# Optimization experiments

Hardware: AMD Instinct MI355X
Metric: run time of the kernel (lower is better)

The kernel has to match this reference:

```python
import jax, jax.numpy as jnp
import numpy as np
import math

NUM_HEADS = 16
HEAD_DIM = 64

def setup_inputs() -> dict:
    key = jax.random.key(0)
    k1, = jax.random.split(key, 1)
    x = jax.random.normal(k1, (4, 4096, NUM_HEADS, HEAD_DIM), dtype=jnp.float32)
    log_amp = jnp.zeros((NUM_HEADS,), dtype=jnp.float32)
    log_decay = jnp.full((NUM_HEADS,), math.log(0.3), dtype=jnp.float32)
    mix_logit = jnp.zeros((NUM_HEADS,), dtype=jnp.float32)
    return {"x": x, "log_amp": log_amp, "log_decay": log_decay, "mix_logit": mix_logit}

def _next_power_of_two(v: int) -> int:
    return 1 << (v - 1).bit_length()

def reference(x, log_amp, log_decay, mix_logit):
    B, L, H, D = x.shape
    n_fft = _next_power_of_two(2 * L)  # 8192 for L=4096
    # b l h d -> b h d l
    xf = jnp.transpose(x, (0, 2, 3, 1)).astype(jnp.float32)
    F = jnp.fft.rfft(xf, n=n_fft, axis=-1)  # [B,H,D,n_fft//2+1] complex64
    freq = jnp.arange(F.shape[-1], dtype=jnp.float32)
    amp = jax.nn.softplus(log_amp)[None, :, None, None]
    decay = jax.nn.softplus(log_decay)[None, :, None, None] + 1e-4
    # minimum-phase power-law filter: |H| = amp/(1+w^2)^(decay/2), phase = -decay*atan(w)
    mag = amp / jnp.power(1.0 + freq * freq, decay * 0.5)
    phase = -decay * jnp.arctan(freq)
    filt = (mag * jnp.cos(phase) + 1j * (mag * jnp.sin(phase))).astype(F.dtype)
    y = jnp.fft.irfft(F * filt, n=n_fft, axis=-1)[..., :L]
    y = jnp.transpose(y, (0, 3, 1, 2)).astype(x.dtype)  # b h d l -> b l h d
    mix = jax.nn.sigmoid(mix_logit)[None, None, :, None]
    return mix * y + (1.0 - mix) * x
```

## Files before the change

kernel.cpp:

```cpp
#include <hip/hip_runtime.h>
#include <math.h>

namespace {
constexpr int kB = 4;
constexpr int kL = 4096;
constexpr int kH = 16;
constexpr int kD = 64;
constexpr int kC = kH * kD;
constexpr int kM = 4096;
constexpr int kN2 = kL / 2;
constexpr int NTH = 256;
constexpr int kTabIters = 9;

__device__ __forceinline__ float2 cmul(float2 a, float2 b) {
  return make_float2(a.x * b.x - a.y * b.y, a.x * b.y + a.y * b.x);
}
__device__ __forceinline__ float2 cadd(float2 a, float2 b) { return make_float2(a.x + b.x, a.y + b.y); }
__device__ __forceinline__ float2 csub(float2 a, float2 b) { return make_float2(a.x - b.x, a.y - b.y); }
__device__ __forceinline__ float2 cconj(float2 a) { return make_float2(a.x, -a.y); }
__device__ __forceinline__ float2 cmuli(float2 a) { return make_float2(-a.y, a.x); }
__device__ __forceinline__ float2 cscale(float2 a, float s) { return make_float2(a.x * s, a.y * s); }

typedef float cplx __attribute__((ext_vector_type(2)));

__device__ __forceinline__ cplx pk_add(cplx a, cplx b) {
  cplx r;
  asm("v_pk_add_f32 %0, %1, %2" : "=v"(r) : "v"(a), "v"(b));
  return r;
}
__device__ __forceinline__ cplx pk_sub(cplx a, cplx b) {
  cplx r;
  asm("v_pk_add_f32 %0, %1, %2 neg_lo:[0,1] neg_hi:[0,1]" : "=v"(r) : "v"(a), "v"(b));
  return r;
}
__device__ __forceinline__ cplx pk_addpi(cplx a, cplx b) {
  cplx r;
  asm("v_pk_add_f32 %0, %1, %2 op_sel:[0,1] op_sel_hi:[1,0] neg_lo:[0,1]" : "=v"(r) : "v"(a), "v"(b));
  return r;
}
__device__ __forceinline__ cplx pk_addmi(cplx a, cplx b) {
  cplx r;
  asm("v_pk_add_f32 %0, %1, %2 op_sel:[0,1] op_sel_hi:[1,0] neg_hi:[0,1]" : "=v"(r) : "v"(a), "v"(b));
  return r;
}
__device__ __forceinline__ cplx pk_cmul(cplx a, cplx b) {
  cplx t, r;
  asm("v_pk_mul_f32 %0, %1, %2 op_sel:[0,0] op_sel_hi:[0,1]" : "=v"(t) : "v"(a), "v"(b));
  asm("v_pk_fma_f32 %0, %1, %2, %3 op_sel:[1,1,0] op_sel_hi:[1,0,1] neg_lo:[0,1,0]"
      : "=v"(r) : "v"(a), "v"(b), "v"(t));
  return r;
}

__device__ __forceinline__ unsigned pkbf(float lo, float hi) {
  unsigned r;
  asm("v_cvt_pk_bf16_f32 %0, %1, %2" : "=v"(r) : "v"(lo), "v"(hi));
  return r;
}
__device__ __forceinline__ cplx unpk(unsigned d) {
  cplx r;
  r.x = __uint_as_float(d << 16);
  r.y = __uint_as_float(d & 0xffff0000u);
  return r;
}

__device__ __forceinline__ unsigned dr4(unsigned p) {
  unsigned r = __brev(p) >> 20;
  return ((r & 0x555u) << 1) | ((r >> 1) & 0x555u);
}
__device__ __forceinline__ unsigned dr16(unsigned p) {
  return ((p & 15u) << 8) | (p & 0xF0u) | (p >> 8);
}
__device__ __forceinline__ int SW(int i) { return i ^ ((i >> 4) & 15); }
#define POS(k) ((((k) & 3) << 2) | ((k) >> 2))

__device__ __forceinline__ int IDX(int i) { return i + (i >> 4); }
constexpr int kZPad = kM + (kM >> 4);

#define TW_TREE(w)                                                            \
  cplx W1 = (w), W2 = pk_cmul(W1, W1), W4 = pk_cmul(W2, W2),                  \
       W8 = pk_cmul(W4, W4);                                                  \
  cplx W3 = pk_cmul(W2, W1), W5 = pk_cmul(W4, W1), W6 = pk_cmul(W4, W2),      \
       W7 = pk_cmul(W4, W3);                                                  \
  cplx W9 = pk_cmul(W8, W1), W10 = pk_cmul(W8, W2), W11 = pk_cmul(W8, W3),    \
       W12 = pk_cmul(W8, W4);                                                 \
  cplx W13 = pk_cmul(W8, W5), W14 = pk_cmul(W8, W6), W15 = pk_cmul(W8, W7);

#define TW_APPLY(r)                                                           \
  r[POS(1)] = pk_cmul(r[POS(1)], W1);   r[POS(2)] = pk_cmul(r[POS(2)], W2);   \
  r[POS(3)] = pk_cmul(r[POS(3)], W3);   r[POS(4)] = pk_cmul(r[POS(4)], W4);   \
  r[POS(5)] = pk_cmul(r[POS(5)], W5);   r[POS(6)] = pk_cmul(r[POS(6)], W6);   \
  r[POS(7)] = pk_cmul(r[POS(7)], W7);   r[POS(8)] = pk_cmul(r[POS(8)], W8);   \
  r[POS(9)] = pk_cmul(r[POS(9)], W9);   r[POS(10)] = pk_cmul(r[POS(10)], W10);\
  r[POS(11)] = pk_cmul(r[POS(11)], W11); r[POS(12)] = pk_cmul(r[POS(12)], W12);\
  r[POS(13)] = pk_cmul(r[POS(13)], W13); r[POS(14)] = pk_cmul(r[POS(14)], W14);\
  r[POS(15)] = pk_cmul(r[POS(15)], W15);

#define TWS_TREE(b0, w)                                                       \
  cplx P2 = pk_cmul(w, w), P4 = pk_cmul(P2, P2), P8 = pk_cmul(P4, P4);        \
  cplx B0 = (b0), B1 = pk_cmul(b0, w), B2 = pk_cmul(B0, P2),                  \
       B3 = pk_cmul(B1, P2);                                                  \
  cplx B4 = pk_cmul(B0, P4), B5 = pk_cmul(B1, P4), B6 = pk_cmul(B2, P4),      \
       B7 = pk_cmul(B3, P4);                                                  \
  cplx B8 = pk_cmul(B0, P8), B9 = pk_cmul(B1, P8), B10 = pk_cmul(B2, P8),     \
       B11 = pk_cmul(B3, P8);                                                 \
  cplx B12 = pk_cmul(B4, P8), B13 = pk_cmul(B5, P8), B14 = pk_cmul(B6, P8),   \
       B15 = pk_cmul(B7, P8);

#define TWS_APPLY(r)                                                          \
  r[POS(0)] = pk_cmul(r[POS(0)], B0);   r[POS(1)] = pk_cmul(r[POS(1)], B1);   \
  r[POS(2)] = pk_cmul(r[POS(2)], B2);   r[POS(3)] = pk_cmul(r[POS(3)], B3);   \
  r[POS(4)] = pk_cmul(r[POS(4)], B4);   r[POS(5)] = pk_cmul(r[POS(5)], B5);   \
  r[POS(6)] = pk_cmul(r[POS(6)], B6);   r[POS(7)] = pk_cmul(r[POS(7)], B7);   \
  r[POS(8)] = pk_cmul(r[POS(8)], B8);   r[POS(9)] = pk_cmul(r[POS(9)], B9);   \
  r[POS(10)] = pk_cmul(r[POS(10)], B10); r[POS(11)] = pk_cmul(r[POS(11)], B11);\
  r[POS(12)] = pk_cmul(r[POS(12)], B12); r[POS(13)] = pk_cmul(r[POS(13)], B13);\
  r[POS(14)] = pk_cmul(r[POS(14)], B14); r[POS(15)] = pk_cmul(r[POS(15)], B15);

__device__ __forceinline__ float2 filt_val(float k, float ampS, float dec) {
  float mag = ampS * __expf(-0.5f * dec * log1pf(k * k));
  float ph = -dec * atanf(k);
  float s, c;
  __sincosf(ph, &s, &c);
  return make_float2(mag * c, mag * s);
}

template <int S, bool HZ>
__device__ __forceinline__ void fft16(cplx r[16]) {
  constexpr float C1 = 0.92387953251128674f;
  constexpr float S1 = 0.38268343236508978f;
  constexpr float R2 = 0.70710678118654752f;
  const float sg = (float)S;
  const cplx Wa = {C1, sg * S1};
  const cplx Wb = {R2, sg * R2};
  const cplx Wc = {S1, sg * C1};
  const cplx Wd = {-R2, sg * R2};
  const cplx We = {-C1, -sg * S1};
#pragma unroll
  for (int n2 = 0; n2 < 4; ++n2) {
    cplx t0, t1, t2, t3;
    if (HZ) {
      t0 = r[n2]; t1 = r[n2]; t2 = r[n2 + 4]; t3 = r[n2 + 4];
    } else {
      cplx a0 = r[n2], a1 = r[n2 + 4], a2 = r[n2 + 8], a3 = r[n2 + 12];
      t0 = pk_add(a0, a2); t1 = pk_sub(a0, a2); t2 = pk_add(a1, a3); t3 = pk_sub(a1, a3);
    }
    cplx u0 = pk_add(t0, t2);
    cplx u2 = pk_sub(t0, t2);
    cplx u1 = (S < 0) ? pk_addmi(t1, t3) : pk_addpi(t1, t3);
    cplx u3 = (S < 0) ? pk_addpi(t1, t3) : pk_addmi(t1, t3);
    if (n2 == 0) { r[0] = u0; r[4] = u1; r[8] = u2; r[12] = u3; }
    if (n2 == 1) { r[1] = u0; r[5] = pk_cmul(u1, Wa); r[9] = pk_cmul(u2, Wb); r[13] = pk_cmul(u3, Wc); }
    if (n2 == 2) {
      r[2] = u0; r[6] = pk_cmul(u1, Wb);
      cplx m;
      if (S < 0) { m.x = u2.y; m.y = -u2.x; } else { m.x = -u2.y; m.y = u2.x; }
      r[10] = m;
      r[14] = pk_cmul(u3, Wd);
    }
    if (n2 == 3) { r[3] = u0; r[7] = pk_cmul(u1, Wc); r[11] = pk_cmul(u2, Wd); r[15] = pk_cmul(u3, We); }
  }
#pragma unroll
  for (int s = 0; s < 4; ++s) {
    cplx b0 = r[4 * s], b1 = r[4 * s + 1], b2 = r[4 * s + 2], b3 = r[4 * s + 3];
    cplx t0 = pk_add(b0, b2), t1 = pk_sub(b0, b2), t2 = pk_add(b1, b3), t3 = pk_sub(b1, b3);
    r[4 * s] = pk_add(t0, t2);
    r[4 * s + 2] = pk_sub(t0, t2);
    r[4 * s + 1] = (S < 0) ? pk_addmi(t1, t3) : pk_addpi(t1, t3);
    r[4 * s + 3] = (S < 0) ? pk_addpi(t1, t3) : pk_addmi(t1, t3);
  }
}

__device__ __forceinline__ void pw_pair(float2 Zk, float2 Zmk, int k, float ampS, float dec,
                                        float2* Wk, float2* Wmk) {
  float2 A = cscale(cadd(Zk, cconj(Zmk)), 0.5f);
  float2 Bv = cscale(csub(Zk, cconj(Zmk)), 0.5f);
  float sn, cs;
  __sincosf(-3.14159265358979323846f * (float)k / (float)kM, &sn, &cs);
  float2 tw = make_float2(cs, sn);
  float2 P = cmuli(cmul(tw, Bv));
  float2 Xk = csub(A, P);
  float2 Xmk = cconj(cadd(A, P));
  float2 Yk = cmul(Xk, filt_val((float)k, ampS, dec));
  float2 Ymk = cmul(Xmk, filt_val((float)(kM - k), ampS, dec));
  float2 Ev = cscale(cadd(Yk, cconj(Ymk)), 0.5f);
  float2 Ov = cscale(cmul(cconj(tw), csub(Yk, cconj(Ymk))), 0.5f);
  float2 iO = cmuli(Ov);
  *Wk = cadd(Ev, iO);
  *Wmk = cconj(csub(Ev, iO));
}
}

__global__ __launch_bounds__(256) void build_table(const float* __restrict__ la,
                                                   const float* __restrict__ ld,
                                                   float2* __restrict__ tab) {
  const int i = blockIdx.x;
  const int h = blockIdx.y;
  const int t = threadIdx.x;
  float av = la[h], dv = ld[h];
  float amp = (av > 20.f) ? av : log1pf(__expf(av));
  float dec = ((dv > 20.f) ? dv : log1pf(__expf(dv))) + 1e-4f;
  float ampS = amp * (1.0f / (float)kM);
  float2 e0 = make_float2(0.f, 0.f), e1 = e0, e2 = e0, e3 = e0;
  const int c = t & 15;
  if (i == 0 && t == 0) {
    float F0 = filt_val(0.f, ampS, dec).x;
    float FM = filt_val((float)kM, ampS, dec).x;
    e0 = make_float2(0.5f * (F0 + FM), 0.5f * (F0 - FM));
    e1 = make_float2(0.5f * (F0 - FM), 0.5f * (F0 + FM));
  } else if (i == 0 && t == 8) {
    e0 = cconj(filt_val((float)(kM / 2), ampS, dec));
  } else if ((i >= 1 && i <= 7) || c < 8) {
    int p = (i << 8) + t;
    int k = (int)dr16((unsigned)p);
    float2 a, b, g, d;
    pw_pair(make_float2(1.f, 0.f), make_float2(0.f, 0.f), k, ampS, dec, &a, &g);
    pw_pair(make_float2(0.f, 0.f), make_float2(1.f, 0.f), k, ampS, dec, &b, &d);
    e0 = a; e1 = b; e2 = g; e3 = d;
  }
  float2* e = tab + ((size_t)(h * kTabIters + i) * 256 + t) * 4;
  e[0] = e0; e[1] = e1; e[2] = e2; e[3] = e3;
}

__global__ __launch_bounds__(256) void transpose_fwd(const float* __restrict__ in,
                                                     unsigned* __restrict__ zout) {
  __shared__ float T[64][33];
  const int b = blockIdx.z;
  const int l0 = blockIdx.x * 64;
  const int c0 = blockIdx.y * 32;
  const float* ib = in + (size_t)b * kL * kC;
  unsigned* ob = zout + (size_t)b * kC * kN2;
  const int tx = threadIdx.x & 31, ty = threadIdx.x >> 5;
#pragma unroll
  for (int i = 0; i < 64; i += 8)
    T[ty + i][tx] = ib[(size_t)(l0 + ty + i) * kC + c0 + tx];
  __syncthreads();
  const int n0 = l0 >> 1;
#pragma unroll
  for (int i = 0; i < 32; i += 8) {
    int c = ty + i;
    ob[(size_t)(c0 + c) * kN2 + n0 + tx] = pkbf(T[2 * tx][c], T[2 * tx + 1][c]);
  }
}

__global__ __launch_bounds__(NTH) void fft_rows(unsigned* __restrict__ zio,
                                                const float2* __restrict__ tab) {
  __shared__ cplx Z[kM];
  const int row = blockIdx.x;
  const int h = (row >> 6) & (kH - 1);
  const int t = threadIdx.x;
  unsigned* zrow = zio + (size_t)row * kN2;

  cplx r[16];
  const int swt = t ^ ((t >> 4) & 15);

  {
    unsigned din[8];
#pragma unroll
    for (int j = 0; j < 8; ++j) din[j] = zrow[t + (j << 8)];
#pragma unroll
    for (int j = 0; j < 8; ++j) r[j] = unpk(din[j]);
    fft16<-1, true>(r);
    float sn, cs;
    __sincosf(-6.283185307179586f * (float)t / 4096.f, &sn, &cs);
    cplx w = {cs, sn};
    TW_TREE(w);
    TW_APPLY(r);
    cplx* Zb = &Z[swt];
#pragma unroll
    for (int k1 = 0; k1 < 16; ++k1) Zb[k1 << 8] = r[POS(k1)];
  }
  __syncthreads();

  {
    const int g = t >> 4, m2 = t & 15;
    const int base = g << 8;
#pragma unroll
    for (int m1 = 0; m1 < 16; ++m1) r[m1] = Z[base + (m1 << 4) + (m2 ^ m1)];
    fft16<-1, false>(r);
    float sn, cs;
    __sincosf(-6.283185307179586f * (float)m2 / 256.f, &sn, &cs);
    cplx w = {cs, sn};
    TW_TREE(w);
    TW_APPLY(r);
#pragma unroll
    for (int j1 = 0; j1 < 16; ++j1) Z[base + (j1 << 4) + (m2 ^ j1)] = r[POS(j1)];
  }
  __syncthreads();

  {
    const int g = t >> 4, j1 = t & 15;
    const int base = (g << 8) + (j1 << 4);
#pragma unroll
    for (int m2 = 0; m2 < 16; ++m2) r[m2] = Z[base + (m2 ^ j1)];
    fft16<-1, false>(r);
#pragma unroll
    for (int j2 = 0; j2 < 16; ++j2) Z[base + (j2 ^ j1)] = r[POS(j2)];
  }
  __syncthreads();

  {
    const int c = t & 15;
    const float4* tpz = (const float4*)(tab + (size_t)h * kTabIters * 256 * 4);
#pragma unroll
    for (int i = 0; i <= 8; ++i) {
      const float4* tp = tpz + ((i << 8) + t) * 2;
      float4 q0 = tp[0], q1 = tp[1];
      if (i == 0 && t == 0) {
        cplx Z0 = Z[0];
        cplx o; o.x = q0.x * Z0.x + q0.y * Z0.y; o.y = q0.z * Z0.x + q0.w * Z0.y;
        Z[0] = o;
      } else if (i == 0 && t == 8) {
        cplx f; f.x = q0.x; f.y = q0.y;
        Z[8] = pk_cmul(f, Z[8]);
      } else if ((i >= 1 && i <= 7) || c < 8) {
        int p = (i << 8) + t;
        int p2 = (i == 0) ? ((t < 16) ? (16 - t) : (271 - t))
                          : (((16 - i) << 8) + (255 - t));
        int sp = SW(p), sp2 = SW(p2);
        cplx Zk = Z[sp], Zmk = Z[sp2];
        cplx e0 = {q0.x, q0.y}, e1 = {q0.z, q0.w};
        cplx e2 = {q1.x, q1.y}, e3 = {q1.z, q1.w};
        cplx cZk = {Zk.x, -Zk.y}, cZmk = {Zmk.x, -Zmk.y};
        Z[sp] = pk_add(pk_cmul(e0, Zk), pk_cmul(e1, cZmk));
        Z[sp2] = pk_add(pk_cmul(e2, cZk), pk_cmul(e3, Zmk));
      }
    }
  }
  __syncthreads();

  {
    const int k1 = t >> 4, j1 = t & 15;
    const int base = (k1 << 8) + (j1 << 4);
#pragma unroll
    for (int j2 = 0; j2 < 16; ++j2) r[j2] = Z[base + (j2 ^ j1)];
    fft16<1, false>(r);
    float sn, cs;
    __sincosf(6.283185307179586f * (float)j1 / 256.f, &sn, &cs);
    cplx w = {cs, sn};
    TW_TREE(w);
    TW_APPLY(r);
#pragma unroll
    for (int m2 = 0; m2 < 16; ++m2) Z[base + (m2 ^ j1)] = r[POS(m2)];
  }
  __syncthreads();

  {
    const int k1 = t >> 4, m2 = t & 15;
#pragma unroll
    for (int j1 = 0; j1 < 16; ++j1) r[j1] = Z[(k1 << 8) + (j1 << 4) + (m2 ^ j1)];
    fft16<1, false>(r);
    float sn, cs;
    __sincosf(6.283185307179586f * (float)(k1 * m2) / 4096.f, &sn, &cs);
    cplx b0 = {cs, sn};
    __sincosf(6.283185307179586f * (float)k1 / 256.f, &sn, &cs);
    cplx w = {cs, sn};
    TWS_TREE(b0, w);
    TWS_APPLY(r);
#pragma unroll
    for (int m1 = 0; m1 < 16; ++m1) Z[(k1 << 8) + (m1 << 4) + (m2 ^ m1)] = r[POS(m1)];
  }
  __syncthreads();

  {
    cplx* Zb = &Z[swt];
#pragma unroll
    for (int k1 = 0; k1 < 16; ++k1) r[k1] = Zb[k1 << 8];
    fft16<1, false>(r);
#pragma unroll
    for (int n1 = 0; n1 < 8; ++n1) {
      cplx v = r[POS(n1)];
      zrow[(n1 << 8) + t] = pkbf(v.x, v.y);
    }
  }
}

__global__ __launch_bounds__(256) void mix_out(const unsigned* __restrict__ zin,
                                               const float* __restrict__ x,
                                               const float* __restrict__ mix_logit,
                                               float* __restrict__ outp) {
  __shared__ float T[64][33];
  const int b = blockIdx.z;
  const int l0 = blockIdx.x * 64;
  const int c0 = blockIdx.y * 32;
  const int h = c0 >> 6;
  const float ml = mix_logit[h];
  const float mix = 1.0f / (1.0f + __expf(-ml));
  const float omix = 1.0f - mix;
  const unsigned* yb = zin + (size_t)b * kC * kN2;
  const float* xb = x + (size_t)b * kL * kC;
  float* ob = outp + (size_t)b * kL * kC;
  const int tx = threadIdx.x & 31, ty = threadIdx.x >> 5;
  const int n0 = l0 >> 1;
#pragma unroll
  for (int i = 0; i < 32; i += 8) {
    int c = ty + i;
    unsigned d = yb[(size_t)(c0 + c) * kN2 + n0 + tx];
    T[2 * tx][c] = __uint_as_float(d << 16);
    T[2 * tx + 1][c] = __uint_as_float(d & 0xffff0000u);
  }
  __syncthreads();
#pragma unroll
  for (int i = 0; i < 64; i += 8) {
    int l = ty + i;
    size_t idx = (size_t)(l0 + l) * kC + c0 + tx;
    ob[idx] = mix * T[l][tx] + omix * xb[idx];
  }
}

__global__ __launch_bounds__(NTH) void fftconv_fallback(
    const float* __restrict__ x, const float* __restrict__ log_amp,
    const float* __restrict__ log_decay, const float* __restrict__ mix_logit,
    float* __restrict__ out) {
  __shared__ float2 Z[kZPad];
  const int row = blockIdx.x;
  const int d = row & (kD - 1);
  const int h = (row >> 6) & (kH - 1);
  const int b = row >> 10;
  const int t = threadIdx.x;
  const size_t rowoff = (size_t)b * kL * kC + (size_t)h * kD + (size_t)d;
  const float* xrow = x + rowoff;
  float* orow = out + rowoff;

  const float av = log_amp[h];
  const float dv = log_decay[h];
  const float amp = (av > 20.f) ? av : log1pf(__expf(av));
  const float dec = ((dv > 20.f) ? dv : log1pf(__expf(dv))) + 1e-4f;
  const float ampS = amp * (1.0f / (float)kM);
  const float ml = mix_logit[h];
  const float mix = 1.0f / (1.0f + __expf(-ml));
  const float omix = 1.0f - mix;

  for (int i = 0; i < kM / NTH; ++i) {
    int n = t + i * NTH;
    float2 z;
    if (n < kL / 2) {
      z.x = xrow[(size_t)(2 * n) * kC];
      z.y = xrow[(size_t)(2 * n + 1) * kC];
    } else {
      z = make_float2(0.f, 0.f);
    }
    Z[IDX(n)] = z;
  }
  __syncthreads();

  for (int Ls = kM; Ls >= 4; Ls >>= 2) {
    const int q = Ls >> 2;
    const float wstep = -6.283185307179586f / (float)Ls;
    for (int i = 0; i < kM / 4 / NTH; ++i) {
      int bt = t + i * NTH;
      int jj = bt & (q - 1);
      int base = ((bt - jj) << 2) + jj;
      float2 a = Z[IDX(base)], bb = Z[IDX(base + q)];
      float2 c = Z[IDX(base + 2 * q)], dd = Z[IDX(base + 3 * q)];
      float2 t0 = cadd(a, c), t1 = csub(a, c), t2 = cadd(bb, dd), t3 = csub(bb, dd);
      float2 u0 = cadd(t0, t2), u2 = csub(t0, t2);
      float2 it3 = cmuli(t3);
      float2 u1 = csub(t1, it3), u3 = cadd(t1, it3);
      float sn, cs;
      __sincosf(wstep * (float)jj, &sn, &cs);
      float2 w1 = make_float2(cs, sn);
      float2 w2 = cmul(w1, w1);
      float2 w3 = cmul(w2, w1);
      Z[IDX(base)] = u0;
      Z[IDX(base + q)] = cmul(u1, w1);
      Z[IDX(base + 2 * q)] = cmul(u2, w2);
      Z[IDX(base + 3 * q)] = cmul(u3, w3);
    }
    __syncthreads();
  }

  for (int i = 0; i <= kM / 2 / NTH; ++i) {
    int k = t + i * NTH;
    if (k > kM / 2) continue;
    if (k == 0) {
      float2 Z0 = Z[IDX(0)];
      float X0 = Z0.x + Z0.y;
      float XM = Z0.x - Z0.y;
      float2 f0 = filt_val(0.f, ampS, dec);
      float2 fM = filt_val((float)kM, ampS, dec);
      float Y0 = X0 * f0.x;
      float YM = XM * fM.x;
      Z[IDX(0)] = make_float2(0.5f * (Y0 + YM), 0.5f * (Y0 - YM));
    } else if (k == kM / 2) {
      unsigned p = dr4(kM / 2);
      float2 Zk = Z[IDX(p)];
      float2 f = filt_val((float)(kM / 2), ampS, dec);
      float2 Y = cmul(cconj(Zk), f);
      Z[IDX(p)] = cconj(Y);
    } else {
      unsigned pk = dr4((unsigned)k), pmk = dr4((unsigned)(kM - k));
      float2 Zk = Z[IDX(pk)], Zmk = Z[IDX(pmk)];
      float2 A = cscale(cadd(Zk, cconj(Zmk)), 0.5f);
      float2 Bv = cscale(csub(Zk, cconj(Zmk)), 0.5f);
      float sn, cs;
      __sincosf(-3.14159265358979323846f * (float)k / (float)kM, &sn, &cs);
      float2 tw = make_float2(cs, sn);
      float2 P = cmuli(cmul(tw, Bv));
      float2 Xk = csub(A, P);
      float2 Xmk = cconj(cadd(A, P));
      float2 Yk = cmul(Xk, filt_val((float)k, ampS, dec));
      float2 Ymk = cmul(Xmk, filt_val((float)(kM - k), ampS, dec));
      float2 Ev = cscale(cadd(Yk, cconj(Ymk)), 0.5f);
      float2 Ov = cscale(cmul(cconj(tw), csub(Yk, cconj(Ymk))), 0.5f);
      float2 iO = cmuli(Ov);
      Z[IDX(pk)] = cadd(Ev, iO);
      Z[IDX(pmk)] = cconj(csub(Ev, iO));
    }
  }
  __syncthreads();

  for (int Ls = 4; Ls <= kM; Ls <<= 2) {
    const int q = Ls >> 2;
    const float wstep = 6.283185307179586f / (float)Ls;
    for (int i = 0; i < kM / 4 / NTH; ++i) {
      int bt = t + i * NTH;
      int jj = bt & (q - 1);
      int base = ((bt - jj) << 2) + jj;
      float sn, cs;
      __sincosf(wstep * (float)jj, &sn, &cs);
      float2 w1 = make_float2(cs, sn);
      float2 w2 = cmul(w1, w1);
      float2 w3 = cmul(w2, w1);
      float2 a = Z[IDX(base)];
      float2 bb = cmul(Z[IDX(base + q)], w1);
      float2 c = cmul(Z[IDX(base + 2 * q)], w2);
      float2 dd = cmul(Z[IDX(base + 3 * q)], w3);
      float2 s0 = cadd(a, c), s1 = csub(a, c), s2 = cadd(bb, dd), s3 = csub(bb, dd);
      float2 is3 = cmuli(s3);
      Z[IDX(base)] = cadd(s0, s2);
      Z[IDX(base + 2 * q)] = csub(s0, s2);
      Z[IDX(base + q)] = cadd(s1, is3);
      Z[IDX(base + 3 * q)] = csub(s1, is3);
    }
    __syncthreads();
  }

  for (int i = 0; i < kL / 2 / NTH; ++i) {
    int n = t + i * NTH;
    float2 w = Z[IDX(n)];
    size_t i0 = (size_t)(2 * n) * kC;
    float x0 = xrow[i0];
    float x1 = xrow[i0 + kC];
    orow[i0] = mix * w.x + omix * x0;
    orow[i0 + kC] = mix * w.y + omix * x1;
  }
}

extern "C" void kernel_launch(void* const* d_in, const int* in_sizes, int n_in,
                              void* d_out, int out_size, void* d_ws, size_t ws_size,
                              hipStream_t stream) {
  const float* x = (const float*)d_in[0];
  const float* la = (const float*)d_in[1];
  const float* ld = (const float*)d_in[2];
  const float* ml = (const float*)d_in[3];
  float* out = (float*)d_out;
  const size_t zbytes = (size_t)kB * kC * kN2 * sizeof(unsigned);
  const size_t tabbytes = (size_t)kH * kTabIters * 256 * 4 * sizeof(float2);
  if (ws_size >= zbytes + tabbytes) {
    unsigned* wsz = (unsigned*)d_ws;
    float2* tab = (float2*)((char*)d_ws + zbytes);
    build_table<<<dim3(kTabIters, kH), dim3(256), 0, stream>>>(la, ld, tab);
    transpose_fwd<<<dim3(kL / 64, kC / 32, kB), dim3(256), 0, stream>>>(x, wsz);
    fft_rows<<<dim3(kB * kC), dim3(NTH), 0, stream>>>(wsz, tab);
    mix_out<<<dim3(kL / 64, kC / 32, kB), dim3(256), 0, stream>>>(wsz, x, ml, out);
  } else {
    fftconv_fallback<<<dim3(kB * kC), dim3(NTH), 0, stream>>>(x, la, ld, ml, out);
  }
}
```

Measured before the change: 97.40 us.

## Fuse last forward FFT pass with spectral filter and first inverse pass

Merges the final forward radix-16 stage, the pointwise filter/real-FFT untangling step and the first inverse stage into one register-resident phase. Each thread now fetches its mirrored partner column straight from shared memory instead of running a separate pass over the spectrum. The table is rebuilt as one float4 per output element, and the LDS swizzle changes to xor with (idx&14) so 16-byte vector loads and stores stay contiguous. This removes one shared-memory round trip, one barrier, and the divergent branchy filter loop. In exchange it adds an extra sync inside the block, more register pressure from holding 16-element P and Wv arrays, and possible bank conflicts from the coarser swizzle.

```diff
diff --git a/kernel.cpp b/kernel.cpp
--- a/kernel.cpp
+++ b/kernel.cpp
@@ -10,7 +10,6 @@
 constexpr int kM = 4096;
 constexpr int kN2 = kL / 2;
 constexpr int NTH = 256;
-constexpr int kTabIters = 9;
 
 __device__ __forceinline__ float2 cmul(float2 a, float2 b) {
   return make_float2(a.x * b.x - a.y * b.y, a.x * b.y + a.y * b.x);
@@ -22,6 +21,7 @@
 __device__ __forceinline__ float2 cscale(float2 a, float s) { return make_float2(a.x * s, a.y * s); }
 
 typedef float cplx __attribute__((ext_vector_type(2)));
+typedef float cplx2 __attribute__((ext_vector_type(4)));
 
 __device__ __forceinline__ cplx pk_add(cplx a, cplx b) {
   cplx r;
@@ -70,7 +70,6 @@
 __device__ __forceinline__ unsigned dr16(unsigned p) {
   return ((p & 15u) << 8) | (p & 0xF0u) | (p >> 8);
 }
-__device__ __forceinline__ int SW(int i) { return i ^ ((i >> 4) & 15); }
 #define POS(k) ((((k) & 3) << 2) | ((k) >> 2))
 
 __device__ __forceinline__ int IDX(int i) { return i + (i >> 4); }
@@ -192,33 +191,33 @@
 
 __global__ __launch_bounds__(256) void build_table(const float* __restrict__ la,
                                                    const float* __restrict__ ld,
-                                                   float2* __restrict__ tab) {
-  const int i = blockIdx.x;
+                                                   float4* __restrict__ tab) {
+  const int j2 = blockIdx.x;
   const int h = blockIdx.y;
   const int t = threadIdx.x;
+  const int k1 = t >> 4, j1 = t & 15;
   float av = la[h], dv = ld[h];
   float amp = (av > 20.f) ? av : log1pf(__expf(av));
   float dec = ((dv > 20.f) ? dv : log1pf(__expf(dv))) + 1e-4f;
   float ampS = amp * (1.0f / (float)kM);
-  float2 e0 = make_float2(0.f, 0.f), e1 = e0, e2 = e0, e3 = e0;
-  const int c = t & 15;
-  if (i == 0 && t == 0) {
+  int p = (k1 << 8) + (j1 << 4) + j2;
+  float2 al, be;
+  if (p == 0) {
     float F0 = filt_val(0.f, ampS, dec).x;
     float FM = filt_val((float)kM, ampS, dec).x;
-    e0 = make_float2(0.5f * (F0 + FM), 0.5f * (F0 - FM));
-    e1 = make_float2(0.5f * (F0 - FM), 0.5f * (F0 + FM));
-  } else if (i == 0 && t == 8) {
-    e0 = cconj(filt_val((float)(kM / 2), ampS, dec));
-  } else if ((i >= 1 && i <= 7) || c < 8) {
-    int p = (i << 8) + t;
+    al = make_float2(0.5f * (F0 + FM), 0.f);
+    be = make_float2(0.f, 0.5f * (F0 - FM));
+  } else if (p == 8) {
+    al = cconj(filt_val((float)(kM / 2), ampS, dec));
+    be = make_float2(0.f, 0.f);
+  } else {
     int k = (int)dr16((unsigned)p);
     float2 a, b, g, d;
     pw_pair(make_float2(1.f, 0.f), make_float2(0.f, 0.f), k, ampS, dec, &a, &g);
     pw_pair(make_float2(0.f, 0.f), make_float2(1.f, 0.f), k, ampS, dec, &b, &d);
-    e0 = a; e1 = b; e2 = g; e3 = d;
-  }
-  float2* e = tab + ((size_t)(h * kTabIters + i) * 256 + t) * 4;
-  e[0] = e0; e[1] = e1; e[2] = e2; e[3] = e3;
+    al = a; be = b;
+  }
+  tab[(((size_t)h * 16 + j2) << 8) + t] = make_float4(al.x, al.y, be.x, be.y);
 }
 
 __global__ __launch_bounds__(256) void transpose_fwd(const float* __restrict__ in,
@@ -243,15 +242,15 @@
 }
 
 __global__ __launch_bounds__(NTH) void fft_rows(unsigned* __restrict__ zio,
-                                                const float2* __restrict__ tab) {
-  __shared__ cplx Z[kM];
+                                                const float4* __restrict__ tab) {
+  __shared__ __align__(16) cplx Z[kM];
   const int row = blockIdx.x;
   const int h = (row >> 6) & (kH - 1);
   const int t = threadIdx.x;
   unsigned* zrow = zio + (size_t)row * kN2;
 
   cplx r[16];
-  const int swt = t ^ ((t >> 4) & 15);
+  const int swt = t ^ ((t >> 4) & 14);
 
   {
     unsigned din[8];
@@ -275,7 +274,7 @@
     const int g = t >> 4, m2 = t & 15;
     const int base = g << 8;
 #pragma unroll
-    for (int m1 = 0; m1 < 16; ++m1) r[m1] = Z[base + (m1 << 4) + (m2 ^ m1)];
+    for (int m1 = 0; m1 < 16; ++m1) r[m1] = Z[base + (m1 << 4) + (m2 ^ (m1 & 14))];
     fft16<-1, false>(r);
     float sn, cs;
     __sincosf(-6.283185307179586f * (float)m2 / 256.f, &sn, &cs);
@@ -283,71 +282,74 @@
     TW_TREE(w);
     TW_APPLY(r);
 #pragma unroll
-    for (int j1 = 0; j1 < 16; ++j1) Z[base + (j1 << 4) + (m2 ^ j1)] = r[POS(j1)];
-  }
-  __syncthreads();
-
-  {
-    const int g = t >> 4, j1 = t & 15;
-    const int base = (g << 8) + (j1 << 4);
-#pragma unroll
-    for (int m2 = 0; m2 < 16; ++m2) r[m2] = Z[base + (m2 ^ j1)];
-    fft16<-1, false>(r);
-#pragma unroll
-    for (int j2 = 0; j2 < 16; ++j2) Z[base + (j2 ^ j1)] = r[POS(j2)];
-  }
-  __syncthreads();
-
-  {
-    const int c = t & 15;
-    const float4* tpz = (const float4*)(tab + (size_t)h * kTabIters * 256 * 4);
-#pragma unroll
-    for (int i = 0; i <= 8; ++i) {
-      const float4* tp = tpz + ((i << 8) + t) * 2;
-      float4 q0 = tp[0], q1 = tp[1];
-      if (i == 0 && t == 0) {
-        cplx Z0 = Z[0];
-        cplx o; o.x = q0.x * Z0.x + q0.y * Z0.y; o.y = q0.z * Z0.x + q0.w * Z0.y;
-        Z[0] = o;
-      } else if (i == 0 && t == 8) {
-        cplx f; f.x = q0.x; f.y = q0.y;
-        Z[8] = pk_cmul(f, Z[8]);
-      } else if ((i >= 1 && i <= 7) || c < 8) {
-        int p = (i << 8) + t;
-        int p2 = (i == 0) ? ((t < 16) ? (16 - t) : (271 - t))
-                          : (((16 - i) << 8) + (255 - t));
-        int sp = SW(p), sp2 = SW(p2);
-        cplx Zk = Z[sp], Zmk = Z[sp2];
-        cplx e0 = {q0.x, q0.y}, e1 = {q0.z, q0.w};
-        cplx e2 = {q1.x, q1.y}, e3 = {q1.z, q1.w};
-        cplx cZk = {Zk.x, -Zk.y}, cZmk = {Zmk.x, -Zmk.y};
-        Z[sp] = pk_add(pk_cmul(e0, Zk), pk_cmul(e1, cZmk));
-        Z[sp2] = pk_add(pk_cmul(e2, cZk), pk_cmul(e3, Zmk));
-      }
-    }
+    for (int j1 = 0; j1 < 16; ++j1) Z[base + (j1 << 4) + (m2 ^ (j1 & 14))] = r[POS(j1)];
   }
   __syncthreads();
 
   {
     const int k1 = t >> 4, j1 = t & 15;
     const int base = (k1 << 8) + (j1 << 4);
-#pragma unroll
-    for (int j2 = 0; j2 < 16; ++j2) r[j2] = Z[base + (j2 ^ j1)];
-    fft16<1, false>(r);
+    const int xo = j1 & 14;
+    cplx2* Zp = (cplx2*)Z;
+
+#pragma unroll
+    for (int q = 0; q < 8; ++q) {
+      cplx2 v = Zp[(base + ((2 * q) ^ xo)) >> 1];
+      r[2 * q].x = v.x; r[2 * q].y = v.y;
+      r[2 * q + 1].x = v.z; r[2 * q + 1].y = v.w;
+    }
+    fft16<-1, false>(r);
+#pragma unroll
+    for (int q = 0; q < 8; ++q) {
+      cplx a = r[POS(2 * q)], b = r[POS(2 * q + 1)];
+      cplx2 v; v.x = a.x; v.y = a.y; v.z = b.x; v.w = b.y;
+      Zp[(base + ((2 * q) ^ xo)) >> 1] = v;
+    }
+    __syncthreads();
+
+    const int base2 = (k1 == 0) ? (((16 - j1) & 15) << 4)
+                                : (((16 - k1) << 8) + ((15 - j1) << 4));
+    const int xo2 = ((k1 == 0) ? ((16 - j1) & 15) : (15 - j1)) & 14;
+    cplx P[16];
+#pragma unroll
+    for (int q = 0; q < 8; ++q) {
+      cplx2 v = Zp[(base2 + ((2 * q) ^ xo2)) >> 1];
+      P[2 * q].x = v.x; P[2 * q].y = v.y;
+      P[2 * q + 1].x = v.z; P[2 * q + 1].y = v.w;
+    }
+    const float4* tb = tab + ((size_t)h << 12) + t;
+    cplx Wv[16];
+    const bool sp = (t == 0);
+#pragma unroll
+    for (int j2 = 0; j2 < 16; ++j2) {
+      float4 cc = tb[j2 << 8];
+      cplx a_; a_.x = cc.x; a_.y = cc.y;
+      cplx b_; b_.x = cc.z; b_.y = cc.w;
+      cplx zm = sp ? P[(16 - j2) & 15] : P[15 - j2];
+      cplx zmc; zmc.x = zm.x; zmc.y = -zm.y;
+      Wv[j2] = pk_add(pk_cmul(a_, r[POS(j2)]), pk_cmul(b_, zmc));
+    }
+    __syncthreads();
+
+    fft16<1, false>(Wv);
     float sn, cs;
     __sincosf(6.283185307179586f * (float)j1 / 256.f, &sn, &cs);
     cplx w = {cs, sn};
     TW_TREE(w);
-    TW_APPLY(r);
-#pragma unroll
-    for (int m2 = 0; m2 < 16; ++m2) Z[base + (m2 ^ j1)] = r[POS(m2)];
+    TW_APPLY(Wv);
+#pragma unroll
+    for (int q = 0; q < 8; ++q) {
+      cplx a = Wv[POS(2 * q)], b = Wv[POS(2 * q + 1)];
+      cplx2 v; v.x = a.x; v.y = a.y; v.z = b.x; v.w = b.y;
+      Zp[(base + ((2 * q) ^ xo)) >> 1] = v;
+    }
   }
   __syncthreads();
 
   {
     const int k1 = t >> 4, m2 = t & 15;
 #pragma unroll
-    for (int j1 = 0; j1 < 16; ++j1) r[j1] = Z[(k1 << 8) + (j1 << 4) + (m2 ^ j1)];
+    for (int j1 = 0; j1 < 16; ++j1) r[j1] = Z[(k1 << 8) + (j1 << 4) + (m2 ^ (j1 & 14))];
     fft16<1, false>(r);
     float sn, cs;
     __sincosf(6.283185307179586f * (float)(k1 * m2) / 4096.f, &sn, &cs);
@@ -357,7 +359,7 @@
     TWS_TREE(b0, w);
     TWS_APPLY(r);
 #pragma unroll
-    for (int m1 = 0; m1 < 16; ++m1) Z[(k1 << 8) + (m1 << 4) + (m2 ^ m1)] = r[POS(m1)];
+    for (int m1 = 0; m1 < 16; ++m1) Z[(k1 << 8) + (m1 << 4) + (m2 ^ (m1 & 14))] = r[POS(m1)];
   }
   __syncthreads();
 
@@ -555,11 +557,11 @@
   const float* ml = (const float*)d_in[3];
   float* out = (float*)d_out;
   const size_t zbytes = (size_t)kB * kC * kN2 * sizeof(unsigned);
-  const size_t tabbytes = (size_t)kH * kTabIters * 256 * 4 * sizeof(float2);
+  const size_t tabbytes = (size_t)kH * 16 * 256 * sizeof(float4);
   if (ws_size >= zbytes + tabbytes) {
     unsigned* wsz = (unsigned*)d_ws;
-    float2* tab = (float2*)((char*)d_ws + zbytes);
-    build_table<<<dim3(kTabIters, kH), dim3(256), 0, stream>>>(la, ld, tab);
+    float4* tab = (float4*)((char*)d_ws + zbytes);
+    build_table<<<dim3(16, kH), dim3(256), 0, stream>>>(la, ld, tab);
     transpose_fwd<<<dim3(kL / 64, kC / 32, kB), dim3(256), 0, stream>>>(x, wsz);
     fft_rows<<<dim3(kB * kC), dim3(NTH), 0, stream>>>(wsz, tab);
     mix_out<<<dim3(kL / 64, kC / 32, kB), dim3(256), 0, stream>>>(wsz, x, ml, out);
```

Result: slower. 135.9 us (+39.5%).

## Fuse filter table build into transpose launch and reuse stage twiddles in inverse FFT

Applied to the files above, without the earlier changes.

Folds the build_table kernel into transpose_fwd as an extra z-slice of blocks, which removes one kernel launch and its serialization gap. In fft_rows, the twiddle powers computed in the second forward stage are kept in registers, and the matching inverse stage reuses them through a conjugate multiply instead of calling sincos again. This adds 15 live complex registers across the pointwise stage, which may raise register pressure and lower occupancy. It also adds 32x16 mostly idle blocks to the transpose grid.

```diff
diff --git a/kernel.cpp b/kernel.cpp
--- a/kernel.cpp
+++ b/kernel.cpp
@@ -47,6 +47,13 @@
   cplx t, r;
   asm("v_pk_mul_f32 %0, %1, %2 op_sel:[0,0] op_sel_hi:[0,1]" : "=v"(t) : "v"(a), "v"(b));
   asm("v_pk_fma_f32 %0, %1, %2, %3 op_sel:[1,1,0] op_sel_hi:[1,0,1] neg_lo:[0,1,0]"
+      : "=v"(r) : "v"(a), "v"(b), "v"(t));
+  return r;
+}
+__device__ __forceinline__ cplx pk_cmulc(cplx a, cplx b) {
+  cplx t, r;
+  asm("v_pk_mul_f32 %0, %1, %2 op_sel:[0,0] op_sel_hi:[0,1] neg_hi:[0,1]" : "=v"(t) : "v"(a), "v"(b));
+  asm("v_pk_fma_f32 %0, %1, %2, %3 op_sel:[1,1,0] op_sel_hi:[1,0,1]"
       : "=v"(r) : "v"(a), "v"(b), "v"(t));
   return r;
 }
@@ -190,40 +197,42 @@
 }
 }
 
-__global__ __launch_bounds__(256) void build_table(const float* __restrict__ la,
-                                                   const float* __restrict__ ld,
-                                                   float2* __restrict__ tab) {
-  const int i = blockIdx.x;
-  const int h = blockIdx.y;
-  const int t = threadIdx.x;
-  float av = la[h], dv = ld[h];
-  float amp = (av > 20.f) ? av : log1pf(__expf(av));
-  float dec = ((dv > 20.f) ? dv : log1pf(__expf(dv))) + 1e-4f;
-  float ampS = amp * (1.0f / (float)kM);
-  float2 e0 = make_float2(0.f, 0.f), e1 = e0, e2 = e0, e3 = e0;
-  const int c = t & 15;
-  if (i == 0 && t == 0) {
-    float F0 = filt_val(0.f, ampS, dec).x;
-    float FM = filt_val((float)kM, ampS, dec).x;
-    e0 = make_float2(0.5f * (F0 + FM), 0.5f * (F0 - FM));
-    e1 = make_float2(0.5f * (F0 - FM), 0.5f * (F0 + FM));
-  } else if (i == 0 && t == 8) {
-    e0 = cconj(filt_val((float)(kM / 2), ampS, dec));
-  } else if ((i >= 1 && i <= 7) || c < 8) {
-    int p = (i << 8) + t;
-    int k = (int)dr16((unsigned)p);
-    float2 a, b, g, d;
-    pw_pair(make_float2(1.f, 0.f), make_float2(0.f, 0.f), k, ampS, dec, &a, &g);
-    pw_pair(make_float2(0.f, 0.f), make_float2(1.f, 0.f), k, ampS, dec, &b, &d);
-    e0 = a; e1 = b; e2 = g; e3 = d;
-  }
-  float2* e = tab + ((size_t)(h * kTabIters + i) * 256 + t) * 4;
-  e[0] = e0; e[1] = e1; e[2] = e2; e[3] = e3;
-}
-
 __global__ __launch_bounds__(256) void transpose_fwd(const float* __restrict__ in,
-                                                     unsigned* __restrict__ zout) {
+                                                     unsigned* __restrict__ zout,
+                                                     const float* __restrict__ la,
+                                                     const float* __restrict__ ld,
+                                                     float2* __restrict__ tab) {
   __shared__ float T[64][33];
+  if (blockIdx.z == kB) {
+    const int i = blockIdx.x;
+    const int h = blockIdx.y;
+    if (i >= kTabIters || h >= kH) return;
+    const int t = threadIdx.x;
+    float av = la[h], dv = ld[h];
+    float amp = (av > 20.f) ? av : log1pf(__expf(av));
+    float dec = ((dv > 20.f) ? dv : log1pf(__expf(dv))) + 1e-4f;
+    float ampS = amp * (1.0f / (float)kM);
+    float2 e0 = make_float2(0.f, 0.f), e1 = e0, e2 = e0, e3 = e0;
+    const int c = t & 15;
+    if (i == 0 && t == 0) {
+      float F0 = filt_val(0.f, ampS, dec).x;
+      float FM = filt_val((float)kM, ampS, dec).x;
+      e0 = make_float2(0.5f * (F0 + FM), 0.5f * (F0 - FM));
+      e1 = make_float2(0.5f * (F0 - FM), 0.5f * (F0 + FM));
+    } else if (i == 0 && t == 8) {
+      e0 = cconj(filt_val((float)(kM / 2), ampS, dec));
+    } else if ((i >= 1 && i <= 7) || c < 8) {
+      int p = (i << 8) + t;
+      int k = (int)dr16((unsigned)p);
+      float2 a, b, g, d;
+      pw_pair(make_float2(1.f, 0.f), make_float2(0.f, 0.f), k, ampS, dec, &a, &g);
+      pw_pair(make_float2(0.f, 0.f), make_float2(1.f, 0.f), k, ampS, dec, &b, &d);
+      e0 = a; e1 = b; e2 = g; e3 = d;
+    }
+    float2* e = tab + ((size_t)(h * kTabIters + i) * 256 + t) * 4;
+    e[0] = e0; e[1] = e1; e[2] = e2; e[3] = e3;
+    return;
+  }
   const int b = blockIdx.z;
   const int l0 = blockIdx.x * 64;
   const int c0 = blockIdx.y * 32;
@@ -252,6 +261,7 @@
 
   cplx r[16];
   const int swt = t ^ ((t >> 4) & 15);
+  cplx H1, H2, H3, H4, H5, H6, H7, H8, H9, H10, H11, H12, H13, H14, H15;
 
   {
     unsigned din[8];
@@ -280,8 +290,18 @@
     float sn, cs;
     __sincosf(-6.283185307179586f * (float)m2 / 256.f, &sn, &cs);
     cplx w = {cs, sn};
-    TW_TREE(w);
-    TW_APPLY(r);
+    H1 = w; H2 = pk_cmul(H1, H1); H4 = pk_cmul(H2, H2); H8 = pk_cmul(H4, H4);
+    H3 = pk_cmul(H2, H1); H5 = pk_cmul(H4, H1); H6 = pk_cmul(H4, H2); H7 = pk_cmul(H4, H3);
+    H9 = pk_cmul(H8, H1); H10 = pk_cmul(H8, H2); H11 = pk_cmul(H8, H3); H12 = pk_cmul(H8, H4);
+    H13 = pk_cmul(H8, H5); H14 = pk_cmul(H8, H6); H15 = pk_cmul(H8, H7);
+    r[POS(1)] = pk_cmul(r[POS(1)], H1);   r[POS(2)] = pk_cmul(r[POS(2)], H2);
+    r[POS(3)] = pk_cmul(r[POS(3)], H3);   r[POS(4)] = pk_cmul(r[POS(4)], H4);
+    r[POS(5)] = pk_cmul(r[POS(5)], H5);   r[POS(6)] = pk_cmul(r[POS(6)], H6);
+    r[POS(7)] = pk_cmul(r[POS(7)], H7);   r[POS(8)] = pk_cmul(r[POS(8)], H8);
+    r[POS(9)] = pk_cmul(r[POS(9)], H9);   r[POS(10)] = pk_cmul(r[POS(10)], H10);
+    r[POS(11)] = pk_cmul(r[POS(11)], H11); r[POS(12)] = pk_cmul(r[POS(12)], H12);
+    r[POS(13)] = pk_cmul(r[POS(13)], H13); r[POS(14)] = pk_cmul(r[POS(14)], H14);
+    r[POS(15)] = pk_cmul(r[POS(15)], H15);
 #pragma unroll
     for (int j1 = 0; j1 < 16; ++j1) Z[base + (j1 << 4) + (m2 ^ j1)] = r[POS(j1)];
   }
@@ -334,11 +354,14 @@
 #pragma unroll
     for (int j2 = 0; j2 < 16; ++j2) r[j2] = Z[base + (j2 ^ j1)];
     fft16<1, false>(r);
-    float sn, cs;
-    __sincosf(6.283185307179586f * (float)j1 / 256.f, &sn, &cs);
-    cplx w = {cs, sn};
-    TW_TREE(w);
-    TW_APPLY(r);
+    r[POS(1)] = pk_cmulc(r[POS(1)], H1);   r[POS(2)] = pk_cmulc(r[POS(2)], H2);
+    r[POS(3)] = pk_cmulc(r[POS(3)], H3);   r[POS(4)] = pk_cmulc(r[POS(4)], H4);
+    r[POS(5)] = pk_cmulc(r[POS(5)], H5);   r[POS(6)] = pk_cmulc(r[POS(6)], H6);
+    r[POS(7)] = pk_cmulc(r[POS(7)], H7);   r[POS(8)] = pk_cmulc(r[POS(8)], H8);
+    r[POS(9)] = pk_cmulc(r[POS(9)], H9);   r[POS(10)] = pk_cmulc(r[POS(10)], H10);
+    r[POS(11)] = pk_cmulc(r[POS(11)], H11); r[POS(12)] = pk_cmulc(r[POS(12)], H12);
+    r[POS(13)] = pk_cmulc(r[POS(13)], H13); r[POS(14)] = pk_cmulc(r[POS(14)], H14);
+    r[POS(15)] = pk_cmulc(r[POS(15)], H15);
 #pragma unroll
     for (int m2 = 0; m2 < 16; ++m2) Z[base + (m2 ^ j1)] = r[POS(m2)];
   }
@@ -559,8 +582,7 @@
   if (ws_size >= zbytes + tabbytes) {
     unsigned* wsz = (unsigned*)d_ws;
     float2* tab = (float2*)((char*)d_ws + zbytes);
-    build_table<<<dim3(kTabIters, kH), dim3(256), 0, stream>>>(la, ld, tab);
-    transpose_fwd<<<dim3(kL / 64, kC / 32, kB), dim3(256), 0, stream>>>(x, wsz);
+    transpose_fwd<<<dim3(kL / 64, kC / 32, kB + 1), dim3(256), 0, stream>>>(x, wsz, la, ld, tab);
     fft_rows<<<dim3(kB * kC), dim3(NTH), 0, stream>>>(wsz, tab);
     mix_out<<<dim3(kL / 64, kC / 32, kB), dim3(256), 0, stream>>>(wsz, x, ml, out);
   } else {
```

After: 95.82 us. Within noise of the previous version (-1.6%).
